# Kernel optimization log

Hardware: AMD Instinct MI355X
Metric: run time of the kernel (lower is better)

The kernel has to match this reference:

```python
import jax, jax.numpy as jnp
import numpy as np

N = 20000
E = 640000
C_IN = 256
C_OUT = 256
K = 2
EPS = 1e-12


def setup_inputs() -> dict:
    key = jax.random.key(0)
    k1, k2, k3, k4, k5 = jax.random.split(key, 5)
    x = jax.random.normal(k1, (N, C_IN), dtype=jnp.float32)
    edge_index = jax.random.randint(k2, (2, E), 0, N, dtype=jnp.int64)
    edge_weights = jax.random.uniform(k3, (E,), dtype=jnp.float32)
    lin_w = jax.random.normal(k4, (C_OUT, C_IN), dtype=jnp.float32) / np.sqrt(C_IN)
    lin_b = jax.random.normal(k5, (C_OUT,), dtype=jnp.float32) * 0.01
    return {"x": x, "edge_index": edge_index, "edge_weights": edge_weights,
            "lin_w": lin_w, "lin_b": lin_b}


def reference(x, edge_index, edge_weights, lin_w, lin_b):
    row, col = edge_index[0], edge_index[1]  # source -> target

    # F.normalize(x, p=2, dim=-1)
    nrm = jnp.sqrt(jnp.sum(x * x, axis=-1, keepdims=True))
    x = x / jnp.maximum(nrm, EPS)

    # gcn_norm with add_self_loops=False (PyG): deg over target nodes
    deg = jax.ops.segment_sum(edge_weights, col, num_segments=N)
    deg_inv_sqrt = jnp.where(deg > 0, 1.0 / jnp.sqrt(deg), 0.0)
    norm = deg_inv_sqrt[row] * edge_weights * deg_inv_sqrt[col]  # [E]

    # K-hop propagation: out[col] += norm * x[row]
    for _ in range(K):
        msgs = norm[:, None] * x[row]                     # [E, C]
        x = jax.ops.segment_sum(msgs, col, num_segments=N)

    # Linear layer of SGConv
    return x @ lin_w.T + lin_b
```

## Files before the change

kernel.cpp:

```cpp
#include <hip/hip_runtime.h>
#include <hip/hip_bf16.h>

#define N_NODES 20000
#define N_EDGES 640000
#define C 256
#define S 96
#define CNTS 16

#define SCATTER_BLOCKS 2500
#define NORM_BLOCKS 10000
#define WCONV_BLOCKS 256

typedef __attribute__((ext_vector_type(8))) short short8;
typedef __attribute__((ext_vector_type(4))) float float4v;

__device__ inline unsigned short f2bf(float f) {
    unsigned u = __float_as_uint(f);
    unsigned r = (u + 0x7fffu + ((u >> 16) & 1u)) >> 16;
    return (unsigned short)r;
}
__device__ inline float bf_lo(unsigned u) { return __uint_as_float(u << 16); }
__device__ inline float bf_hi(unsigned u) { return __uint_as_float(u & 0xffff0000u); }

__global__ __launch_bounds__(256) void fused_pre_kernel(
        const int* __restrict__ ei, const float* __restrict__ w,
        const float* __restrict__ x, const float* __restrict__ lw,
        int* __restrict__ cnt, unsigned* __restrict__ csr,
        unsigned* __restrict__ xs32, unsigned short* __restrict__ Wb) {
    int b = blockIdx.x;
    int t = threadIdx.x;
    if (b < SCATTER_BLOCKS) {
        __shared__ int okw[4];
        unsigned long long m = __ballot(ei[2 * t + 1] == 0);
        if ((t & 63) == 0) okw[t >> 6] = (m == 0xFFFFFFFFFFFFFFFFull) ? 1 : 0;
        __syncthreads();
        int flag = okw[0] & okw[1] & okw[2] & okw[3];
        int e = b * 256 + t;
        int r, c;
        if (flag) { r = ei[2 * e]; c = ei[2 * (N_EDGES + e)]; }
        else      { r = ei[e];     c = ei[N_EDGES + e]; }
        int pos = atomicAdd(&cnt[c * CNTS], 1);
        if (pos < S) csr[c * S + pos] = (unsigned)r | ((unsigned)f2bf(w[e]) << 16);
    } else if (b < SCATTER_BLOCKS + NORM_BLOCKS) {
        int half = t >> 7;
        int tt = t & 127;
        int i = (b - SCATTER_BLOCKS) * 2 + half;
        float2 v = ((const float2*)x)[(size_t)i * 128 + tt];
        float ss = v.x * v.x + v.y * v.y;
        #pragma unroll
        for (int o = 32; o > 0; o >>= 1) ss += __shfl_down(ss, o, 64);
        __shared__ float wsum[4];
        if ((t & 63) == 0) wsum[t >> 6] = ss;
        __syncthreads();
        float tot = wsum[half * 2] + wsum[half * 2 + 1];
        float inv = 1.0f / fmaxf(sqrtf(tot), 1e-12f);
        xs32[(size_t)i * 128 + tt] =
            (unsigned)f2bf(v.x * inv) | ((unsigned)f2bf(v.y * inv) << 16);
    } else {
        int idx = (b - SCATTER_BLOCKS - NORM_BLOCKS) * 256 + t;
        Wb[idx] = f2bf(lw[idx]);
    }
}

__global__ void deg_dis_kernel(const unsigned* __restrict__ csr, const int* __restrict__ cnt,
                               float* __restrict__ dis) {
    int wv = threadIdx.x >> 6;
    int lane = threadIdx.x & 63;
    int i = blockIdx.x * 4 + wv;
    int n = cnt[i * CNTS];
    if (n > S) n = S;
    float s = 0.0f;
    for (int b = lane; b < n; b += 64)
        s += bf_hi(__builtin_nontemporal_load(&csr[i * S + b]));
    #pragma unroll
    for (int o = 32; o > 0; o >>= 1) s += __shfl_down(s, o, 64);
    if (lane == 0) dis[i] = (s > 0.0f) ? rsqrtf(s) : 0.0f;
}

template <int POW, int SRC_DIS>
__global__ __launch_bounds__(256) void gather_kernel(const int* __restrict__ cnt,
                                                     const unsigned* __restrict__ csr,
                                                     const float* __restrict__ dis,
                                                     const unsigned* __restrict__ in,
                                                     unsigned* __restrict__ out) {
    __shared__ int ls_all[4][S];
    __shared__ float lw_all[4][S];
    int wvi = threadIdx.x >> 6;
    int lane = threadIdx.x & 63;
    int i = blockIdx.x * 4 + wvi;
    int n = cnt[i * CNTS];
    if (n > S) n = S;
    int* ls = ls_all[wvi];
    float* lw = lw_all[wvi];
    if (lane < n) {
        unsigned p = __builtin_nontemporal_load(&csr[i * S + lane]);
        int s = (int)(p & 0xffffu);
        float wv = bf_hi(p);
        if (SRC_DIS) wv *= dis[s];
        ls[lane] = s; lw[lane] = wv;
    }
    if (lane + 64 < n) {
        unsigned p = __builtin_nontemporal_load(&csr[i * S + lane + 64]);
        int s = (int)(p & 0xffffu);
        float wv = bf_hi(p);
        if (SRC_DIS) wv *= dis[s];
        ls[lane + 64] = s; lw[lane + 64] = wv;
    }
    __builtin_amdgcn_wave_barrier();

    const uint2* inr = (const uint2*)in;
    float a0 = 0.f, a1 = 0.f, a2 = 0.f, a3 = 0.f;
    int j = 0;
    for (; j + 4 <= n; j += 4) {
        int s0 = ls[j], s1 = ls[j + 1], s2 = ls[j + 2], s3 = ls[j + 3];
        float w0 = lw[j], w1 = lw[j + 1], w2 = lw[j + 2], w3 = lw[j + 3];
        uint2 v0 = inr[(size_t)s0 * 64 + lane];
        uint2 v1 = inr[(size_t)s1 * 64 + lane];
        uint2 v2 = inr[(size_t)s2 * 64 + lane];
        uint2 v3 = inr[(size_t)s3 * 64 + lane];
        a0 += w0 * bf_lo(v0.x); a1 += w0 * bf_hi(v0.x);
        a2 += w0 * bf_lo(v0.y); a3 += w0 * bf_hi(v0.y);
        a0 += w1 * bf_lo(v1.x); a1 += w1 * bf_hi(v1.x);
        a2 += w1 * bf_lo(v1.y); a3 += w1 * bf_hi(v1.y);
        a0 += w2 * bf_lo(v2.x); a1 += w2 * bf_hi(v2.x);
        a2 += w2 * bf_lo(v2.y); a3 += w2 * bf_hi(v2.y);
        a0 += w3 * bf_lo(v3.x); a1 += w3 * bf_hi(v3.x);
        a2 += w3 * bf_lo(v3.y); a3 += w3 * bf_hi(v3.y);
    }
    for (; j < n; j++) {
        int s = ls[j]; float wv = lw[j];
        uint2 v = inr[(size_t)s * 64 + lane];
        a0 += wv * bf_lo(v.x); a1 += wv * bf_hi(v.x);
        a2 += wv * bf_lo(v.y); a3 += wv * bf_hi(v.y);
    }
    float d = dis[i];
    float sc = (POW == 2) ? d * d : d;
    unsigned long long r =
        (unsigned long long)((unsigned)f2bf(a0 * sc) | ((unsigned)f2bf(a1 * sc) << 16)) |
        ((unsigned long long)((unsigned)f2bf(a2 * sc) | ((unsigned)f2bf(a3 * sc) << 16)) << 32);
    __builtin_nontemporal_store(r, (unsigned long long*)out + (size_t)i * 64 + lane);
}

__global__ __launch_bounds__(256) void gemm_kernel(const unsigned short* __restrict__ h,
                                                   const unsigned short* __restrict__ Wb,
                                                   const float* __restrict__ b,
                                                   float* __restrict__ out) {
    int wv = threadIdx.x >> 6;
    int lane = threadIdx.x & 63;
    int m = lane & 15;
    int q = lane >> 4;
    int rowbase = blockIdx.x * 64 + wv * 16;
    int rowA = rowbase + m;
    if (rowA > N_NODES - 1) rowA = N_NODES - 1;
    float4v acc[16];
    #pragma unroll
    for (int nt = 0; nt < 16; nt++) acc[nt] = (float4v){0.f, 0.f, 0.f, 0.f};
    #pragma unroll
    for (int kt = 0; kt < 8; kt++) {
        int kb = kt * 32 + q * 8;
        short8 a = *(const short8*)(h + (size_t)rowA * C + kb);
        #pragma unroll
        for (int nt = 0; nt < 16; nt++) {
            short8 bb = *(const short8*)(Wb + (nt * 16 + m) * C + kb);
            acc[nt] = __builtin_amdgcn_mfma_f32_16x16x32_bf16(a, bb, acc[nt], 0, 0, 0);
        }
    }
    #pragma unroll
    for (int nt = 0; nt < 16; nt++) {
        int col = nt * 16 + m;
        float bias = b[col];
        #pragma unroll
        for (int r = 0; r < 4; r++) {
            int ro = rowbase + q * 4 + r;
            if (ro < N_NODES)
                __builtin_nontemporal_store(acc[nt][r] + bias, &out[(size_t)ro * C + col]);
        }
    }
}

extern "C" void kernel_launch(void* const* d_in, const int* in_sizes, int n_in,
                              void* d_out, int out_size, void* d_ws, size_t ws_size,
                              hipStream_t stream) {
    const float* x  = (const float*)d_in[0];
    const int*   ei = (const int*)d_in[1];
    const float* w  = (const float*)d_in[2];
    const float* lw = (const float*)d_in[3];
    const float* lb = (const float*)d_in[4];
    float* out = (float*)d_out;

    char* ws = (char*)d_ws;
    size_t off = 0;
    auto alloc = [&](size_t bytes) -> void* {
        void* p = ws + off;
        off = (off + bytes + 255) & ~(size_t)255;
        return p;
    };
    unsigned* bufA   = (unsigned*)alloc((size_t)N_NODES * 128 * 4);
    unsigned* bufB   = (unsigned*)alloc((size_t)N_NODES * 128 * 4);
    float* dis       = (float*)alloc((size_t)N_NODES * 4);
    int*   cnt       = (int*)alloc((size_t)N_NODES * CNTS * 4);
    unsigned* csr    = (unsigned*)alloc((size_t)N_NODES * S * 4);
    unsigned short* Wb = (unsigned short*)alloc((size_t)C * C * 2);
    (void)ws_size; (void)in_sizes; (void)n_in; (void)out_size;

    hipMemsetAsync(cnt, 0, (size_t)N_NODES * CNTS * 4, stream);

    fused_pre_kernel<<<SCATTER_BLOCKS + NORM_BLOCKS + WCONV_BLOCKS, 256, 0, stream>>>(
        ei, w, x, lw, cnt, csr, bufA, Wb);
    deg_dis_kernel<<<N_NODES / 4, 256, 0, stream>>>(csr, cnt, dis);
    gather_kernel<2, 1><<<N_NODES / 4, 256, 0, stream>>>(cnt, csr, dis, bufA, bufB);
    gather_kernel<1, 0><<<N_NODES / 4, 256, 0, stream>>>(cnt, csr, dis, bufB, bufA);
    gemm_kernel<<<(N_NODES + 63) / 64, 256, 0, stream>>>(
        (const unsigned short*)bufA, Wb, lb, out);
}
```

Measured before the change: 224.1 us.

## Split feature dimension into four channel chunks for cache-local gather

The bf16 feature buffers now use a chunked layout: four slabs of 64 channels each, laid out node-major. Each gather block handles one chunk, and each wave's two halves process alternate edges, combined at the end with a shuffle. The aim is a per-pass working set of about 2.5MB per chunk, so random row gathers hit L2/MALL more often. In exchange the grid is four times larger, CSR and dis reads are repeated per chunk, and each lane's gather load is narrower; the GEMM A-load and the normalize store are adapted to the new layout.

```diff
diff --git a/kernel.cpp b/kernel.cpp
--- a/kernel.cpp
+++ b/kernel.cpp
@@ -10,6 +10,9 @@
 #define SCATTER_BLOCKS 2500
 #define NORM_BLOCKS 10000
 #define WCONV_BLOCKS 256
+
+#define NCHUNK 4
+#define CHUNK_BLOCKS (N_NODES / 4)
 
 typedef __attribute__((ext_vector_type(8))) short short8;
 typedef __attribute__((ext_vector_type(4))) float float4v;
@@ -54,7 +57,7 @@
         __syncthreads();
         float tot = wsum[half * 2] + wsum[half * 2 + 1];
         float inv = 1.0f / fmaxf(sqrtf(tot), 1e-12f);
-        xs32[(size_t)i * 128 + tt] =
+        xs32[(size_t)(tt >> 5) * (N_NODES * 32) + (size_t)i * 32 + (tt & 31)] =
             (unsigned)f2bf(v.x * inv) | ((unsigned)f2bf(v.y * inv) << 16);
     } else {
         int idx = (b - SCATTER_BLOCKS - NORM_BLOCKS) * 256 + t;
@@ -83,62 +86,68 @@
                                                      const float* __restrict__ dis,
                                                      const unsigned* __restrict__ in,
                                                      unsigned* __restrict__ out) {
-    __shared__ int ls_all[4][S];
-    __shared__ float lw_all[4][S];
+    __shared__ uint2 st_all[4][S + 1];
     int wvi = threadIdx.x >> 6;
     int lane = threadIdx.x & 63;
-    int i = blockIdx.x * 4 + wvi;
+    int chunk = blockIdx.x / CHUNK_BLOCKS;
+    int i = (blockIdx.x % CHUNK_BLOCKS) * 4 + wvi;
     int n = cnt[i * CNTS];
     if (n > S) n = S;
-    int* ls = ls_all[wvi];
-    float* lw = lw_all[wvi];
+    uint2* st = st_all[wvi];
     if (lane < n) {
         unsigned p = __builtin_nontemporal_load(&csr[i * S + lane]);
-        int s = (int)(p & 0xffffu);
+        unsigned s = p & 0xffffu;
         float wv = bf_hi(p);
         if (SRC_DIS) wv *= dis[s];
-        ls[lane] = s; lw[lane] = wv;
+        st[lane] = make_uint2(s << 7, __float_as_uint(wv));
     }
     if (lane + 64 < n) {
         unsigned p = __builtin_nontemporal_load(&csr[i * S + lane + 64]);
-        int s = (int)(p & 0xffffu);
+        unsigned s = p & 0xffffu;
         float wv = bf_hi(p);
         if (SRC_DIS) wv *= dis[s];
-        ls[lane + 64] = s; lw[lane + 64] = wv;
-    }
+        st[lane + 64] = make_uint2(s << 7, __float_as_uint(wv));
+    }
+    if ((n & 1) && lane == 0) st[n] = make_uint2(0u, 0u);
     __builtin_amdgcn_wave_barrier();
 
-    const uint2* inr = (const uint2*)in;
-    float a0 = 0.f, a1 = 0.f, a2 = 0.f, a3 = 0.f;
+    int half = lane >> 5;
+    unsigned hb = (unsigned)(lane & 31) << 2;
+    const char* base = (const char*)in + (size_t)chunk * (N_NODES * 128);
+    float a0 = 0.f, a1 = 0.f;
+    int nup = n + (n & 1);
     int j = 0;
-    for (; j + 4 <= n; j += 4) {
-        int s0 = ls[j], s1 = ls[j + 1], s2 = ls[j + 2], s3 = ls[j + 3];
-        float w0 = lw[j], w1 = lw[j + 1], w2 = lw[j + 2], w3 = lw[j + 3];
-        uint2 v0 = inr[(size_t)s0 * 64 + lane];
-        uint2 v1 = inr[(size_t)s1 * 64 + lane];
-        uint2 v2 = inr[(size_t)s2 * 64 + lane];
-        uint2 v3 = inr[(size_t)s3 * 64 + lane];
-        a0 += w0 * bf_lo(v0.x); a1 += w0 * bf_hi(v0.x);
-        a2 += w0 * bf_lo(v0.y); a3 += w0 * bf_hi(v0.y);
-        a0 += w1 * bf_lo(v1.x); a1 += w1 * bf_hi(v1.x);
-        a2 += w1 * bf_lo(v1.y); a3 += w1 * bf_hi(v1.y);
-        a0 += w2 * bf_lo(v2.x); a1 += w2 * bf_hi(v2.x);
-        a2 += w2 * bf_lo(v2.y); a3 += w2 * bf_hi(v2.y);
-        a0 += w3 * bf_lo(v3.x); a1 += w3 * bf_hi(v3.x);
-        a2 += w3 * bf_lo(v3.y); a3 += w3 * bf_hi(v3.y);
-    }
-    for (; j < n; j++) {
-        int s = ls[j]; float wv = lw[j];
-        uint2 v = inr[(size_t)s * 64 + lane];
-        a0 += wv * bf_lo(v.x); a1 += wv * bf_hi(v.x);
-        a2 += wv * bf_lo(v.y); a3 += wv * bf_hi(v.y);
-    }
-    float d = dis[i];
-    float sc = (POW == 2) ? d * d : d;
-    unsigned long long r =
-        (unsigned long long)((unsigned)f2bf(a0 * sc) | ((unsigned)f2bf(a1 * sc) << 16)) |
-        ((unsigned long long)((unsigned)f2bf(a2 * sc) | ((unsigned)f2bf(a3 * sc) << 16)) << 32);
-    __builtin_nontemporal_store(r, (unsigned long long*)out + (size_t)i * 64 + lane);
+    for (; j + 8 <= nup; j += 8) {
+        uint2 e0 = st[j + half];
+        uint2 e1 = st[j + 2 + half];
+        uint2 e2 = st[j + 4 + half];
+        uint2 e3 = st[j + 6 + half];
+        unsigned v0 = *(const unsigned*)(base + (e0.x + hb));
+        unsigned v1 = *(const unsigned*)(base + (e1.x + hb));
+        unsigned v2 = *(const unsigned*)(base + (e2.x + hb));
+        unsigned v3 = *(const unsigned*)(base + (e3.x + hb));
+        float w0 = __uint_as_float(e0.y), w1 = __uint_as_float(e1.y);
+        float w2 = __uint_as_float(e2.y), w3 = __uint_as_float(e3.y);
+        a0 += w0 * bf_lo(v0); a1 += w0 * bf_hi(v0);
+        a0 += w1 * bf_lo(v1); a1 += w1 * bf_hi(v1);
+        a0 += w2 * bf_lo(v2); a1 += w2 * bf_hi(v2);
+        a0 += w3 * bf_lo(v3); a1 += w3 * bf_hi(v3);
+    }
+    for (; j < nup; j += 2) {
+        uint2 e = st[j + half];
+        unsigned v = *(const unsigned*)(base + (e.x + hb));
+        float w = __uint_as_float(e.y);
+        a0 += w * bf_lo(v); a1 += w * bf_hi(v);
+    }
+    a0 += __shfl_down(a0, 32, 64);
+    a1 += __shfl_down(a1, 32, 64);
+    if (lane < 32) {
+        float d = dis[i];
+        float sc = (POW == 2) ? d * d : d;
+        unsigned r = (unsigned)f2bf(a0 * sc) | ((unsigned)f2bf(a1 * sc) << 16);
+        __builtin_nontemporal_store(
+            r, out + (size_t)chunk * (N_NODES * 32) + (size_t)i * 32 + lane);
+    }
 }
 
 __global__ __launch_bounds__(256) void gemm_kernel(const unsigned short* __restrict__ h,
@@ -158,7 +167,9 @@
     #pragma unroll
     for (int kt = 0; kt < 8; kt++) {
         int kb = kt * 32 + q * 8;
-        short8 a = *(const short8*)(h + (size_t)rowA * C + kb);
+        const unsigned short* ap =
+            h + (size_t)(kb >> 6) * (N_NODES * 64) + (size_t)rowA * 64 + (kb & 63);
+        short8 a = *(const short8*)ap;
         #pragma unroll
         for (int nt = 0; nt < 16; nt++) {
             short8 bb = *(const short8*)(Wb + (nt * 16 + m) * C + kb);
@@ -208,8 +219,8 @@
     fused_pre_kernel<<<SCATTER_BLOCKS + NORM_BLOCKS + WCONV_BLOCKS, 256, 0, stream>>>(
         ei, w, x, lw, cnt, csr, bufA, Wb);
     deg_dis_kernel<<<N_NODES / 4, 256, 0, stream>>>(csr, cnt, dis);
-    gather_kernel<2, 1><<<N_NODES / 4, 256, 0, stream>>>(cnt, csr, dis, bufA, bufB);
-    gather_kernel<1, 0><<<N_NODES / 4, 256, 0, stream>>>(cnt, csr, dis, bufB, bufA);
+    gather_kernel<2, 1><<<NCHUNK * CHUNK_BLOCKS, 256, 0, stream>>>(cnt, csr, dis, bufA, bufB);
+    gather_kernel<1, 0><<<NCHUNK * CHUNK_BLOCKS, 256, 0, stream>>>(cnt, csr, dis, bufB, bufA);
     gemm_kernel<<<(N_NODES + 63) / 64, 256, 0, stream>>>(
         (const unsigned short*)bufA, Wb, lb, out);
 }
```

Measured after the change: 246.5 us. 10.0% more time.

## Split wave into two half-waves gathering 16-byte rows with padded edge lists

Applied to the files above, without the earlier changes.

The gather kernel now has each half-wave process alternating neighbours. Every lane loads 16 bytes (8 bf16 values) instead of 8, so the wave issues twice as many independent row fetches per iteration, and the two halves are combined with a shuffle at the end. Neighbour index (pre-shifted to a byte offset) and weight are packed into one uint2 in LDS. The list is padded to a multiple of 8 with zero-weight entries pointing at row 0, which removes the remainder loop at the cost of some wasted loads. The degree kernel also writes a capped per-node count as a byte array, so the gather reads that instead of the strided int counter.

```diff
diff --git a/kernel.cpp b/kernel.cpp
--- a/kernel.cpp
+++ b/kernel.cpp
@@ -13,6 +13,7 @@
 
 typedef __attribute__((ext_vector_type(8))) short short8;
 typedef __attribute__((ext_vector_type(4))) float float4v;
+typedef __attribute__((ext_vector_type(4))) unsigned uint4v;
 
 __device__ inline unsigned short f2bf(float f) {
     unsigned u = __float_as_uint(f);
@@ -21,6 +22,7 @@
 }
 __device__ inline float bf_lo(unsigned u) { return __uint_as_float(u << 16); }
 __device__ inline float bf_hi(unsigned u) { return __uint_as_float(u & 0xffff0000u); }
+__device__ inline float bf_hi_raw(unsigned u) { return __uint_as_float(u); }
 
 __global__ __launch_bounds__(256) void fused_pre_kernel(
         const int* __restrict__ ei, const float* __restrict__ w,
@@ -63,82 +65,102 @@
 }
 
 __global__ void deg_dis_kernel(const unsigned* __restrict__ csr, const int* __restrict__ cnt,
-                               float* __restrict__ dis) {
+                               float* __restrict__ dis, unsigned char* __restrict__ ncap) {
     int wv = threadIdx.x >> 6;
     int lane = threadIdx.x & 63;
     int i = blockIdx.x * 4 + wv;
     int n = cnt[i * CNTS];
     if (n > S) n = S;
     float s = 0.0f;
-    for (int b = lane; b < n; b += 64)
-        s += bf_hi(__builtin_nontemporal_load(&csr[i * S + b]));
+    if (lane < n) s = bf_hi(__builtin_nontemporal_load(&csr[i * S + lane]));
+    if (lane + 64 < n) s += bf_hi(__builtin_nontemporal_load(&csr[i * S + lane + 64]));
     #pragma unroll
     for (int o = 32; o > 0; o >>= 1) s += __shfl_down(s, o, 64);
-    if (lane == 0) dis[i] = (s > 0.0f) ? rsqrtf(s) : 0.0f;
+    if (lane == 0) {
+        dis[i] = (s > 0.0f) ? rsqrtf(s) : 0.0f;
+        ncap[i] = (unsigned char)n;
+    }
 }
 
 template <int POW, int SRC_DIS>
-__global__ __launch_bounds__(256) void gather_kernel(const int* __restrict__ cnt,
+__global__ __launch_bounds__(256) void gather_kernel(const unsigned char* __restrict__ ncap,
                                                      const unsigned* __restrict__ csr,
                                                      const float* __restrict__ dis,
                                                      const unsigned* __restrict__ in,
                                                      unsigned* __restrict__ out) {
-    __shared__ int ls_all[4][S];
-    __shared__ float lw_all[4][S];
+    __shared__ uint2 st_all[4][S];
     int wvi = threadIdx.x >> 6;
     int lane = threadIdx.x & 63;
     int i = blockIdx.x * 4 + wvi;
-    int n = cnt[i * CNTS];
-    if (n > S) n = S;
-    int* ls = ls_all[wvi];
-    float* lw = lw_all[wvi];
+    int n = ncap[i];
+    int nup = (n + 7) & ~7;
+    uint2* st = st_all[wvi];
     if (lane < n) {
         unsigned p = __builtin_nontemporal_load(&csr[i * S + lane]);
-        int s = (int)(p & 0xffffu);
+        unsigned s = p & 0xffffu;
         float wv = bf_hi(p);
         if (SRC_DIS) wv *= dis[s];
-        ls[lane] = s; lw[lane] = wv;
+        st[lane] = make_uint2(s << 9, __float_as_uint(wv));
     }
     if (lane + 64 < n) {
         unsigned p = __builtin_nontemporal_load(&csr[i * S + lane + 64]);
-        int s = (int)(p & 0xffffu);
+        unsigned s = p & 0xffffu;
         float wv = bf_hi(p);
         if (SRC_DIS) wv *= dis[s];
-        ls[lane + 64] = s; lw[lane + 64] = wv;
+        st[lane + 64] = make_uint2(s << 9, __float_as_uint(wv));
+    }
+    {
+        int k = n + lane;
+        if (k < nup) st[k] = make_uint2(0u, 0u);
     }
     __builtin_amdgcn_wave_barrier();
 
-    const uint2* inr = (const uint2*)in;
-    float a0 = 0.f, a1 = 0.f, a2 = 0.f, a3 = 0.f;
-    int j = 0;
-    for (; j + 4 <= n; j += 4) {
-        int s0 = ls[j], s1 = ls[j + 1], s2 = ls[j + 2], s3 = ls[j + 3];
-        float w0 = lw[j], w1 = lw[j + 1], w2 = lw[j + 2], w3 = lw[j + 3];
-        uint2 v0 = inr[(size_t)s0 * 64 + lane];
-        uint2 v1 = inr[(size_t)s1 * 64 + lane];
-        uint2 v2 = inr[(size_t)s2 * 64 + lane];
-        uint2 v3 = inr[(size_t)s3 * 64 + lane];
-        a0 += w0 * bf_lo(v0.x); a1 += w0 * bf_hi(v0.x);
-        a2 += w0 * bf_lo(v0.y); a3 += w0 * bf_hi(v0.y);
-        a0 += w1 * bf_lo(v1.x); a1 += w1 * bf_hi(v1.x);
-        a2 += w1 * bf_lo(v1.y); a3 += w1 * bf_hi(v1.y);
-        a0 += w2 * bf_lo(v2.x); a1 += w2 * bf_hi(v2.x);
-        a2 += w2 * bf_lo(v2.y); a3 += w2 * bf_hi(v2.y);
-        a0 += w3 * bf_lo(v3.x); a1 += w3 * bf_hi(v3.x);
-        a2 += w3 * bf_lo(v3.y); a3 += w3 * bf_hi(v3.y);
-    }
-    for (; j < n; j++) {
-        int s = ls[j]; float wv = lw[j];
-        uint2 v = inr[(size_t)s * 64 + lane];
-        a0 += wv * bf_lo(v.x); a1 += wv * bf_hi(v.x);
-        a2 += wv * bf_lo(v.y); a3 += wv * bf_hi(v.y);
-    }
-    float d = dis[i];
-    float sc = (POW == 2) ? d * d : d;
-    unsigned long long r =
-        (unsigned long long)((unsigned)f2bf(a0 * sc) | ((unsigned)f2bf(a1 * sc) << 16)) |
-        ((unsigned long long)((unsigned)f2bf(a2 * sc) | ((unsigned)f2bf(a3 * sc) << 16)) << 32);
-    __builtin_nontemporal_store(r, (unsigned long long*)out + (size_t)i * 64 + lane);
+    int grp = lane >> 5;
+    unsigned hb = (unsigned)(lane & 31) << 4;
+    const char* base = (const char*)in;
+    float2 c0 = {0.f, 0.f}, c1 = {0.f, 0.f}, c2 = {0.f, 0.f}, c3 = {0.f, 0.f};
+    for (int j = 0; j < nup; j += 8) {
+        uint2 e0 = st[j + grp];
+        uint2 e1 = st[j + 2 + grp];
+        uint2 e2 = st[j + 4 + grp];
+        uint2 e3 = st[j + 6 + grp];
+        uint4v v0 = *(const uint4v*)(base + (e0.x + hb));
+        uint4v v1 = *(const uint4v*)(base + (e1.x + hb));
+        uint4v v2 = *(const uint4v*)(base + (e2.x + hb));
+        uint4v v3 = *(const uint4v*)(base + (e3.x + hb));
+        float w0 = __uint_as_float(e0.y), w1 = __uint_as_float(e1.y);
+        float w2 = __uint_as_float(e2.y), w3 = __uint_as_float(e3.y);
+        c0.x += w0 * bf_lo(v0.x); c0.y += w0 * bf_hi_raw(v0.x);
+        c1.x += w0 * bf_lo(v0.y); c1.y += w0 * bf_hi_raw(v0.y);
+        c2.x += w0 * bf_lo(v0.z); c2.y += w0 * bf_hi_raw(v0.z);
+        c3.x += w0 * bf_lo(v0.w); c3.y += w0 * bf_hi_raw(v0.w);
+        c0.x += w1 * bf_lo(v1.x); c0.y += w1 * bf_hi_raw(v1.x);
+        c1.x += w1 * bf_lo(v1.y); c1.y += w1 * bf_hi_raw(v1.y);
+        c2.x += w1 * bf_lo(v1.z); c2.y += w1 * bf_hi_raw(v1.z);
+        c3.x += w1 * bf_lo(v1.w); c3.y += w1 * bf_hi_raw(v1.w);
+        c0.x += w2 * bf_lo(v2.x); c0.y += w2 * bf_hi_raw(v2.x);
+        c1.x += w2 * bf_lo(v2.y); c1.y += w2 * bf_hi_raw(v2.y);
+        c2.x += w2 * bf_lo(v2.z); c2.y += w2 * bf_hi_raw(v2.z);
+        c3.x += w2 * bf_lo(v2.w); c3.y += w2 * bf_hi_raw(v2.w);
+        c0.x += w3 * bf_lo(v3.x); c0.y += w3 * bf_hi_raw(v3.x);
+        c1.x += w3 * bf_lo(v3.y); c1.y += w3 * bf_hi_raw(v3.y);
+        c2.x += w3 * bf_lo(v3.z); c2.y += w3 * bf_hi_raw(v3.z);
+        c3.x += w3 * bf_lo(v3.w); c3.y += w3 * bf_hi_raw(v3.w);
+    }
+    c0.x += __shfl_down(c0.x, 32, 64); c0.y += __shfl_down(c0.y, 32, 64);
+    c1.x += __shfl_down(c1.x, 32, 64); c1.y += __shfl_down(c1.y, 32, 64);
+    c2.x += __shfl_down(c2.x, 32, 64); c2.y += __shfl_down(c2.y, 32, 64);
+    c3.x += __shfl_down(c3.x, 32, 64); c3.y += __shfl_down(c3.y, 32, 64);
+    if (lane < 32) {
+        float d = dis[i];
+        float sc = (POW == 2) ? d * d : d;
+        uint4v r;
+        r.x = (unsigned)f2bf(c0.x * sc) | ((unsigned)f2bf(c0.y * sc) << 16);
+        r.y = (unsigned)f2bf(c1.x * sc) | ((unsigned)f2bf(c1.y * sc) << 16);
+        r.z = (unsigned)f2bf(c2.x * sc) | ((unsigned)f2bf(c2.y * sc) << 16);
+        r.w = (unsigned)f2bf(c3.x * sc) | ((unsigned)f2bf(c3.y * sc) << 16);
+        __builtin_nontemporal_store(r, (uint4v*)(out + (size_t)i * 128) + lane);
+    }
 }
 
 __global__ __launch_bounds__(256) void gemm_kernel(const unsigned short* __restrict__ h,
@@ -201,15 +223,16 @@
     int*   cnt       = (int*)alloc((size_t)N_NODES * CNTS * 4);
     unsigned* csr    = (unsigned*)alloc((size_t)N_NODES * S * 4);
     unsigned short* Wb = (unsigned short*)alloc((size_t)C * C * 2);
+    unsigned char* ncap = (unsigned char*)alloc((size_t)N_NODES);
     (void)ws_size; (void)in_sizes; (void)n_in; (void)out_size;
 
-    hipMemsetAsync(cnt, 0, (size_t)N_NODES * CNTS * 4, stream);
+    (void)hipMemsetAsync(cnt, 0, (size_t)N_NODES * CNTS * 4, stream);
 
     fused_pre_kernel<<<SCATTER_BLOCKS + NORM_BLOCKS + WCONV_BLOCKS, 256, 0, stream>>>(
         ei, w, x, lw, cnt, csr, bufA, Wb);
-    deg_dis_kernel<<<N_NODES / 4, 256, 0, stream>>>(csr, cnt, dis);
-    gather_kernel<2, 1><<<N_NODES / 4, 256, 0, stream>>>(cnt, csr, dis, bufA, bufB);
-    gather_kernel<1, 0><<<N_NODES / 4, 256, 0, stream>>>(cnt, csr, dis, bufB, bufA);
+    deg_dis_kernel<<<N_NODES / 4, 256, 0, stream>>>(csr, cnt, dis, ncap);
+    gather_kernel<2, 1><<<N_NODES / 4, 256, 0, stream>>>(ncap, csr, dis, bufA, bufB);
+    gather_kernel<1, 0><<<N_NODES / 4, 256, 0, stream>>>(ncap, csr, dis, bufB, bufA);
     gemm_kernel<<<(N_NODES + 63) / 64, 256, 0, stream>>>(
         (const unsigned short*)bufA, Wb, lb, out);
 }
```

Result: no change. 221.3 us (-1.3%).
